# Performance work log

Hardware: AMD Instinct MI355X
Metric: run time of the kernel (lower is better)

## Reference

```python
import jax, jax.numpy as jnp
import numpy as np

D_MODEL = 1024
NUM_HEADS = 16
HEAD_DIM = D_MODEL // NUM_HEADS
THETA = 10000.0
BATCH, SEQ = 2, 2048


def rope(x, token_positions):
    # x: [b, h, s, d]; token_positions: [s]
    d = x.shape[-1]
    freqs = 1.0 / THETA ** (jnp.arange(0, d, 2, dtype=jnp.float32)[: d // 2] / d)
    ang = token_positions.astype(jnp.float32)[:, None] * freqs[None, :]  # [s, d/2]
    cos, sin = jnp.cos(ang), jnp.sin(ang)
    xr = x.reshape(*x.shape[:-1], d // 2, 2)
    x_even, x_odd = xr[..., 0], xr[..., 1]
    out_even = x_even * cos - x_odd * sin
    out_odd = x_even * sin + x_odd * cos
    return jnp.stack([out_even, out_odd], axis=-1).reshape(x.shape)


def setup_inputs() -> dict:
    key = jax.random.key(0)
    ks = jax.random.split(key, 5)
    std = np.sqrt(2.0 / (D_MODEL + D_MODEL))
    mk = lambda k: (jax.random.truncated_normal(k, -3.0, 3.0, (D_MODEL, D_MODEL), jnp.float32) * std)
    return {
        "x": jax.random.normal(ks[0], (BATCH, SEQ, D_MODEL), jnp.float32),
        "Wq": mk(ks[1]),
        "Wk": mk(ks[2]),
        "Wv": mk(ks[3]),
        "Wo": mk(ks[4]),
        "casual_mask": jnp.tril(jnp.ones((SEQ, SEQ), dtype=bool)),
        "token_positions": jnp.arange(SEQ, dtype=jnp.int32),
    }


def reference(x, Wq, Wk, Wv, Wo, casual_mask, token_positions):
    b, s, _ = x.shape
    split = lambda t: t.reshape(b, s, NUM_HEADS, HEAD_DIM).transpose(0, 2, 1, 3)
    q = split(x @ Wq.T)  # [b, h, s, d]
    k = split(x @ Wk.T)
    v = split(x @ Wv.T)
    q = rope(q, token_positions)
    k = rope(k, token_positions)
    scores = jnp.einsum("bhqd,bhkd->bhqk", q, k) / np.sqrt(HEAD_DIM)
    scores = jnp.where(casual_mask, scores, -jnp.inf)
    probs = jax.nn.softmax(scores, axis=-1)
    out = jnp.einsum("bhqk,bhkd->bhqd", probs, v)
    out = out.transpose(0, 2, 1, 3).reshape(b, s, D_MODEL)
    return out @ Wo.T
```

## Files before the change

kernel.cpp:

```cpp
#include <hip/hip_runtime.h>
#include <hip/hip_bf16.h>

#define SEQ_LEN 2048
#define NBATCH 2
#define DM 1024
#define NH 16
#define HD 64
#define NR (NBATCH * SEQ_LEN)
#define NQKV (3 * DM)
#define LDQK 2048

typedef __attribute__((ext_vector_type(8))) short bf16x8;
typedef __attribute__((ext_vector_type(4))) float f32x4;

__device__ __forceinline__ short f2b(float f) {
    __hip_bfloat16 h = __float2bfloat16(f);
    return *reinterpret_cast<short*>(&h);
}
__device__ __forceinline__ float b2f(short s) {
    union { unsigned u; float f; } x;
    x.u = ((unsigned)(unsigned short)s) << 16;
    return x.f;
}

__device__ __forceinline__ void gload_lds16(const void* g, void* l) {
    __builtin_amdgcn_global_load_lds(
        (const __attribute__((address_space(1))) unsigned int*)g,
        (__attribute__((address_space(3))) unsigned int*)l, 16, 0, 0);
}

__global__ __launch_bounds__(256) void cvt_all(
    const float* __restrict__ x,  const float* __restrict__ wq,
    const float* __restrict__ wk, const float* __restrict__ wv,
    const float* __restrict__ wo,
    __hip_bfloat16* __restrict__ xb, __hip_bfloat16* __restrict__ wqkvb,
    __hip_bfloat16* __restrict__ wob) {
    int id = blockIdx.x;
    const float* src; __hip_bfloat16* dst;
    if (id < 4096) { src = x + (size_t)id * 1024; dst = xb + (size_t)id * 1024; }
    else {
        int k = id - 4096, seg = k >> 10;
        size_t off = (size_t)(k & 1023) * 1024;
        if      (seg == 0) { src = wq + off; dst = wqkvb + off; }
        else if (seg == 1) { src = wk + off; dst = wqkvb + (1u << 20) + off; }
        else if (seg == 2) { src = wv + off; dst = wqkvb + (2u << 20) + off; }
        else               { src = wo + off; dst = wob + off; }
    }
    int i = threadIdx.x * 4;
    float4 v = *(const float4*)(src + i);
    dst[i + 0] = __float2bfloat16(v.x);
    dst[i + 1] = __float2bfloat16(v.y);
    dst[i + 2] = __float2bfloat16(v.z);
    dst[i + 3] = __float2bfloat16(v.w);
}

__device__ __forceinline__ void store_c(float* p, float v) { *p = v; }
__device__ __forceinline__ void store_c(__hip_bfloat16* p, float v) {
    *p = __float2bfloat16(v);
}

template <typename CT, bool FUSED>
__global__ __launch_bounds__(256) void gemm128(
    const __hip_bfloat16* __restrict__ A,
    const __hip_bfloat16* __restrict__ B,
    CT* __restrict__ C, int K, int ldc,
    __hip_bfloat16* __restrict__ Vtg) {
    __shared__ __hip_bfloat16 As[128 * 32];
    __shared__ __hip_bfloat16 Bs[128 * 32];
    const int t    = threadIdx.x;
    const int wave = t >> 6;
    const int lane = t & 63;
    const int quad = lane >> 4;
    const int l16  = lane & 15;
    const int wy = wave >> 1, wx = wave & 1;
    const int m0 = blockIdx.x * 128, n0 = blockIdx.y * 128;

    const int r0 = wave * 32 + (lane >> 2);
    const int c0 = (lane & 3) * 8;
    const __hip_bfloat16* Ag0 = A + (size_t)(m0 + r0) * K + c0;
    const __hip_bfloat16* Ag1 = Ag0 + (size_t)16 * K;
    const __hip_bfloat16* Bg0 = B + (size_t)(n0 + r0) * K + c0;
    const __hip_bfloat16* Bg1 = Bg0 + (size_t)16 * K;
    __hip_bfloat16* lA0 = &As[r0 * 32 + c0];
    __hip_bfloat16* lA1 = &As[(r0 + 16) * 32 + c0];
    __hip_bfloat16* lB0 = &Bs[r0 * 32 + c0];
    __hip_bfloat16* lB1 = &Bs[(r0 + 16) * 32 + c0];

    f32x4 acc[4][4];
#pragma unroll
    for (int i = 0; i < 4; i++)
#pragma unroll
        for (int j = 0; j < 4; j++) acc[i][j] = (f32x4){0.f, 0.f, 0.f, 0.f};

    for (int k0 = 0; k0 < K; k0 += 32) {
        __syncthreads();
        gload_lds16(Ag0 + k0, lA0);
        gload_lds16(Ag1 + k0, lA1);
        gload_lds16(Bg0 + k0, lB0);
        gload_lds16(Bg1 + k0, lB1);
        __syncthreads();

        bf16x8 af[4], bfr[4];
#pragma unroll
        for (int rb = 0; rb < 4; rb++)
            af[rb] = *(const bf16x8*)&As[(wy * 64 + rb * 16 + l16) * 32 + quad * 8];
#pragma unroll
        for (int cb = 0; cb < 4; cb++)
            bfr[cb] = *(const bf16x8*)&Bs[(wx * 64 + cb * 16 + l16) * 32 + quad * 8];
#pragma unroll
        for (int rb = 0; rb < 4; rb++)
#pragma unroll
            for (int cb = 0; cb < 4; cb++)
                acc[rb][cb] = __builtin_amdgcn_mfma_f32_16x16x32_bf16(
                    af[rb], bfr[cb], acc[rb][cb], 0, 0, 0);
    }

    if (!FUSED || blockIdx.y < 16) {
#pragma unroll
        for (int rb = 0; rb < 4; rb++)
#pragma unroll
            for (int r = 0; r < 4; r++) {
                size_t ro = (size_t)(m0 + wy * 64 + rb * 16 + quad * 4 + r) * ldc;
#pragma unroll
                for (int cb = 0; cb < 4; cb++)
                    store_c(&C[ro + n0 + wx * 64 + cb * 16 + l16], acc[rb][cb][r]);
            }
    } else {
#pragma unroll
        for (int rb = 0; rb < 4; rb++) {
            int row0 = m0 + wy * 64 + rb * 16 + quad * 4;
            int bb = row0 >> 11, ss = row0 & (SEQ_LEN - 1);
#pragma unroll
            for (int cb = 0; cb < 4; cb++) {
                int vcol = n0 + wx * 64 + cb * 16 + l16 - 2048;
                int hh = vcol >> 6, dd = vcol & 63;
                ushort4 u;
                u.x = (unsigned short)f2b(acc[rb][cb][0]);
                u.y = (unsigned short)f2b(acc[rb][cb][1]);
                u.z = (unsigned short)f2b(acc[rb][cb][2]);
                u.w = (unsigned short)f2b(acc[rb][cb][3]);
                *(ushort4*)(Vtg + ((size_t)(bb * NH + hh) * HD + dd) * SEQ_LEN + ss) = u;
            }
        }
    }
}

__global__ __launch_bounds__(256) void rope_kernel(
    __hip_bfloat16* __restrict__ QK, const int* __restrict__ pos) {
    int idx = blockIdx.x * 256 + threadIdx.x;
    int row  = idx >> 8;
    int tcol = idx & 255;
    int col0 = tcol * 8;
    int head = col0 >> 6;
    int i0   = (col0 & 63) >> 1;
    float p  = (float)pos[row & (SEQ_LEN - 1)];
    float scale = (head < NH) ? 0.125f : 1.0f;
    __hip_bfloat16* ptr = QK + (size_t)row * LDQK + col0;
    bf16x8 v = *(const bf16x8*)ptr;
    bf16x8 o;
#pragma unroll
    for (int k = 0; k < 4; k++) {
        float fr = __expf(-(float)(2 * (i0 + k)) * (9.210340371976184f / 64.0f));
        float ang = p * fr;
        float sn = sinf(ang), cs = cosf(ang);
        float e  = b2f(v[2 * k]);
        float od = b2f(v[2 * k + 1]);
        o[2 * k]     = f2b((e * cs - od * sn) * scale);
        o[2 * k + 1] = f2b((e * sn + od * cs) * scale);
    }
    *(bf16x8*)ptr = o;
}

__global__ __launch_bounds__(512) void attn_kernel(
    const __hip_bfloat16* __restrict__ QK,
    const __hip_bfloat16* __restrict__ Vtg,
    __hip_bfloat16* __restrict__ O) {
    __shared__ __hip_bfloat16 Ks[2][64 * 64];
    __shared__ __hip_bfloat16 Vs[2][64 * 64];
    __shared__ short Ps[128][72];

    const int t    = threadIdx.x;
    const int wave = t >> 6;
    const int lane = t & 63;
    const int quad = lane >> 4;
    const int l16  = lane & 15;
    const int pairIdx = blockIdx.x >> 5;
    const int hb      = blockIdx.x & 31;
    const int h       = hb & 15;
    const int b       = hb >> 4;

    const int sr  = t >> 3;
    const int scs = (t & 7) ^ (sr & 7);

    const __hip_bfloat16* kbase = QK + (size_t)(b * SEQ_LEN) * LDQK + DM + h * HD;
    const __hip_bfloat16* vbase = Vtg + (size_t)((b * NH + h) * HD) * SEQ_LEN;

#define STAGE(BUF, KT)                                                          \
    {                                                                           \
        gload_lds16(kbase + (size_t)((KT) * 64 + sr) * LDQK + scs * 8,          \
                    (char*)&Ks[BUF][0] + t * 16);                               \
        gload_lds16(vbase + (size_t)sr * SEQ_LEN + (KT) * 64 + scs * 8,         \
                    (char*)&Vs[BUF][0] + t * 16);                               \
    }

#define LDS_FRAG(BASE, RR, G)                                                   \
    (*(const bf16x8*)((const char*)(BASE) + (RR) * 128 + ((((G) ^ ((RR) & 7))) << 4)))

#define TRIP(BUF, KT)                                                           \
    {                                                                           \
        bf16x8 kf[4][2];                                                        \
        _Pragma("unroll") for (int kb = 0; kb < 4; kb++) {                      \
            int rr = kb * 16 + l16;                                             \
            kf[kb][0] = LDS_FRAG(Ks[BUF], rr, quad);                            \
            kf[kb][1] = LDS_FRAG(Ks[BUF], rr, quad + 4);                        \
        }                                                                       \
        f32x4 s[4];                                                             \
        _Pragma("unroll") for (int kb = 0; kb < 4; kb++) {                      \
            f32x4 z = {0.f, 0.f, 0.f, 0.f};                                     \
            z = __builtin_amdgcn_mfma_f32_16x16x32_bf16(qf0, kf[kb][0], z, 0, 0, 0); \
            z = __builtin_amdgcn_mfma_f32_16x16x32_bf16(qf1, kf[kb][1], z, 0, 0, 0); \
            s[kb] = z;                                                          \
        }                                                                       \
        if ((KT) == ktd) {                \
            _Pragma("unroll") for (int kb = 0; kb < 4; kb++) {                  \
                int key = (KT) * 64 + kb * 16 + l16;                            \
                _Pragma("unroll") for (int r = 0; r < 4; r++) {                 \
                    int rowg = row0 + quad * 4 + r;                             \
                    if (key > rowg) s[kb][r] = -1e30f;                          \
                }                                                               \
            }                                                                   \
        }                                                                       \
        _Pragma("unroll") for (int r = 0; r < 4; r++) {                         \
            float p0 = __expf(s[0][r]);                                         \
            float p1 = __expf(s[1][r]);                                         \
            float p2 = __expf(s[2][r]);                                         \
            float p3 = __expf(s[3][r]);                                         \
            l_p[r] += (p0 + p1) + (p2 + p3);                                    \
            int prow = wave * 16 + quad * 4 + r;                                \
            Ps[prow][ 0 + l16] = f2b(p0);                                       \
            Ps[prow][16 + l16] = f2b(p1);                                       \
            Ps[prow][32 + l16] = f2b(p2);                                       \
            Ps[prow][48 + l16] = f2b(p3);                                       \
        }                                                                       \
        bf16x8 pf0 = *(const bf16x8*)&Ps[wave * 16 + l16][quad * 8];            \
        bf16x8 pf1 = *(const bf16x8*)&Ps[wave * 16 + l16][32 + quad * 8];       \
        _Pragma("unroll") for (int db = 0; db < 4; db++) {                      \
            int rr = db * 16 + l16;                                             \
            bf16x8 vf0 = LDS_FRAG(Vs[BUF], rr, quad);                           \
            bf16x8 vf1 = LDS_FRAG(Vs[BUF], rr, quad + 4);                       \
            o[db] = __builtin_amdgcn_mfma_f32_16x16x32_bf16(pf0, vf0, o[db], 0, 0, 0); \
            o[db] = __builtin_amdgcn_mfma_f32_16x16x32_bf16(pf1, vf1, o[db], 0, 0, 0); \
        }                                                                       \
    }

#define FINALIZE()                                                              \
    {                                                                           \
        _Pragma("unroll") for (int r = 0; r < 4; r++) {                         \
            float rs = l_p[r];                                                  \
            rs += __shfl_xor(rs, 1);                                            \
            rs += __shfl_xor(rs, 2);                                            \
            rs += __shfl_xor(rs, 4);                                            \
            rs += __shfl_xor(rs, 8);                                            \
            float inv = 1.0f / rs;                                              \
            size_t ro = (size_t)(b * SEQ_LEN + row0 + quad * 4 + r) * DM + h * HD; \
            O[ro +  0 + l16] = __float2bfloat16(o[0][r] * inv);                 \
            O[ro + 16 + l16] = __float2bfloat16(o[1][r] * inv);                 \
            O[ro + 32 + l16] = __float2bfloat16(o[2][r] * inv);                 \
            O[ro + 48 + l16] = __float2bfloat16(o[3][r] * inv);                 \
        }                                                                       \
    }

    const int qtB = 15 - pairIdx;
    const int n0t = 2 * qtB + 2;

    int row0 = qtB * 128 + wave * 16;
    int ktd  = row0 >> 6;
    bf16x8 qf0, qf1;
    {
        const __hip_bfloat16* qp =
            QK + (size_t)(b * SEQ_LEN + row0 + l16) * LDQK + h * HD + quad * 8;
        qf0 = *(const bf16x8*)qp;
        qf1 = *(const bf16x8*)(qp + 32);
    }
    f32x4 o[4];
    float l_p[4];
#pragma unroll
    for (int r = 0; r < 4; r++) { o[r] = (f32x4){0.f, 0.f, 0.f, 0.f}; l_p[r] = 0.f; }

    STAGE(0, 0);
    for (int i = 0; i < 34; ++i) {
        const int buf = i & 1;
        __syncthreads();
        if (i + 1 < 34) {
            int inext = i + 1;
            int ktn = (inext < n0t) ? inext : inext - n0t;
            STAGE(buf ^ 1, ktn);
        }
        const int kt = (i < n0t) ? i : i - n0t;
        if (kt <= ktd) TRIP(buf, kt);
        if (i == n0t - 1) {
            FINALIZE();
            row0 = pairIdx * 128 + wave * 16;
            ktd  = row0 >> 6;
            const __hip_bfloat16* qp =
                QK + (size_t)(b * SEQ_LEN + row0 + l16) * LDQK + h * HD + quad * 8;
            qf0 = *(const bf16x8*)qp;
            qf1 = *(const bf16x8*)(qp + 32);
#pragma unroll
            for (int r = 0; r < 4; r++) { o[r] = (f32x4){0.f, 0.f, 0.f, 0.f}; l_p[r] = 0.f; }
        }
    }
    FINALIZE();
#undef STAGE
#undef LDS_FRAG
#undef TRIP
#undef FINALIZE
}

extern "C" void kernel_launch(void* const* d_in, const int* in_sizes, int n_in,
                              void* d_out, int out_size, void* d_ws, size_t ws_size,
                              hipStream_t stream) {
    const float* x  = (const float*)d_in[0];
    const float* Wq = (const float*)d_in[1];
    const float* Wk = (const float*)d_in[2];
    const float* Wv = (const float*)d_in[3];
    const float* Wo = (const float*)d_in[4];
    const int* pos = (const int*)d_in[6];
    float* out = (float*)d_out;

    char* w = (char*)d_ws;
    const size_t MiB = 1024 * 1024;
    __hip_bfloat16* xb    = (__hip_bfloat16*)(w + 0 * MiB);
    __hip_bfloat16* Ab    = (__hip_bfloat16*)(w + 0 * MiB);
    __hip_bfloat16* Wqkvb = (__hip_bfloat16*)(w + 8 * MiB);
    __hip_bfloat16* Wob   = (__hip_bfloat16*)(w + 14 * MiB);
    __hip_bfloat16* QKb   = (__hip_bfloat16*)(w + 16 * MiB);
    __hip_bfloat16* Vtg   = (__hip_bfloat16*)(w + 32 * MiB);

    cvt_all<<<8192, 256, 0, stream>>>(x, Wq, Wk, Wv, Wo, xb, Wqkvb, Wob);

    gemm128<__hip_bfloat16, true><<<dim3(NR / 128, NQKV / 128), 256, 0, stream>>>(
        xb, Wqkvb, QKb, DM, LDQK, Vtg);

    rope_kernel<<<NR * LDQK / 8 / 256, 256, 0, stream>>>(QKb, pos);

    attn_kernel<<<256, 512, 0, stream>>>(QKb, Vtg, Ab);

    gemm128<float, false><<<dim3(NR / 128, DM / 128), 256, 0, stream>>>(
        Ab, Wob, out, DM, DM, nullptr);
}
```

Before: 211.8 us.

## Fuse RoPE into QKV GEMM epilogue and restructure attention into 64-row tiles

Applies RoPE and the query scale inside the QKV GEMM epilogue, using a lane shuffle to fetch the paired element, and deletes the separate rope kernel along with its read and write of the QK buffer. The attention kernel changes from 256 blocks of 512 threads, each handling a paired 128-row tile, to 1024 blocks of 256 threads, each handling one 64-row query tile with heaviest tiles scheduled first. It also wraps the MFMA sections in s_setprio hints. The risks are extra sincos work and shuffles in the GEMM epilogue, and load imbalance from dropping the tile pairing, which the larger grid is meant to absorb.

```diff
diff --git a/kernel.cpp b/kernel.cpp
--- a/kernel.cpp
+++ b/kernel.cpp
@@ -64,7 +64,7 @@
     const __hip_bfloat16* __restrict__ A,
     const __hip_bfloat16* __restrict__ B,
     CT* __restrict__ C, int K, int ldc,
-    __hip_bfloat16* __restrict__ Vtg) {
+    __hip_bfloat16* __restrict__ Vtg, const int* __restrict__ pos) {
     __shared__ __hip_bfloat16 As[128 * 32];
     __shared__ __hip_bfloat16 Bs[128 * 32];
     const int t    = threadIdx.x;
@@ -116,6 +116,31 @@
     }
 
     if (!FUSED || blockIdx.y < 16) {
+        if constexpr (FUSED) {
+            const float sc = (blockIdx.y < 8) ? 0.125f : 1.0f;
+            float fr[4];
+#pragma unroll
+            for (int cb = 0; cb < 4; cb++) {
+                int i = ((cb * 16 + l16) & 63) >> 1;
+                fr[cb] = __expf(-(float)(2 * i) * (9.210340371976184f / 64.0f));
+            }
+            const float par = (l16 & 1) ? 1.f : -1.f;
+#pragma unroll
+            for (int rb = 0; rb < 4; rb++)
+#pragma unroll
+                for (int r = 0; r < 4; r++) {
+                    int row = m0 + wy * 64 + rb * 16 + quad * 4 + r;
+                    float p = (float)pos[row & (SEQ_LEN - 1)];
+#pragma unroll
+                    for (int cb = 0; cb < 4; cb++) {
+                        float sn, cs;
+                        __sincosf(p * fr[cb], &sn, &cs);
+                        float v  = acc[rb][cb][r];
+                        float pt = __shfl_xor(v, 1);
+                        acc[rb][cb][r] = (v * cs + par * pt * sn) * sc;
+                    }
+                }
+        }
 #pragma unroll
         for (int rb = 0; rb < 4; rb++)
 #pragma unroll
@@ -145,49 +170,26 @@
     }
 }
 
-__global__ __launch_bounds__(256) void rope_kernel(
-    __hip_bfloat16* __restrict__ QK, const int* __restrict__ pos) {
-    int idx = blockIdx.x * 256 + threadIdx.x;
-    int row  = idx >> 8;
-    int tcol = idx & 255;
-    int col0 = tcol * 8;
-    int head = col0 >> 6;
-    int i0   = (col0 & 63) >> 1;
-    float p  = (float)pos[row & (SEQ_LEN - 1)];
-    float scale = (head < NH) ? 0.125f : 1.0f;
-    __hip_bfloat16* ptr = QK + (size_t)row * LDQK + col0;
-    bf16x8 v = *(const bf16x8*)ptr;
-    bf16x8 o;
-#pragma unroll
-    for (int k = 0; k < 4; k++) {
-        float fr = __expf(-(float)(2 * (i0 + k)) * (9.210340371976184f / 64.0f));
-        float ang = p * fr;
-        float sn = sinf(ang), cs = cosf(ang);
-        float e  = b2f(v[2 * k]);
-        float od = b2f(v[2 * k + 1]);
-        o[2 * k]     = f2b((e * cs - od * sn) * scale);
-        o[2 * k + 1] = f2b((e * sn + od * cs) * scale);
-    }
-    *(bf16x8*)ptr = o;
-}
-
-__global__ __launch_bounds__(512) void attn_kernel(
+__global__ __launch_bounds__(256) void attn_kernel(
     const __hip_bfloat16* __restrict__ QK,
     const __hip_bfloat16* __restrict__ Vtg,
     __hip_bfloat16* __restrict__ O) {
     __shared__ __hip_bfloat16 Ks[2][64 * 64];
     __shared__ __hip_bfloat16 Vs[2][64 * 64];
-    __shared__ short Ps[128][72];
+    __shared__ short Ps[64][72];
 
     const int t    = threadIdx.x;
     const int wave = t >> 6;
     const int lane = t & 63;
     const int quad = lane >> 4;
     const int l16  = lane & 15;
-    const int pairIdx = blockIdx.x >> 5;
-    const int hb      = blockIdx.x & 31;
-    const int h       = hb & 15;
-    const int b       = hb >> 4;
+    const int id  = blockIdx.x;
+    const int qt  = 31 - (id >> 5);
+    const int hb  = id & 31;
+    const int h   = hb & 15;
+    const int b   = hb >> 4;
+
+    const int row0 = qt * 64 + wave * 16;
 
     const int sr  = t >> 3;
     const int scs = (t & 7) ^ (sr & 7);
@@ -199,8 +201,12 @@
     {                                                                           \
         gload_lds16(kbase + (size_t)((KT) * 64 + sr) * LDQK + scs * 8,          \
                     (char*)&Ks[BUF][0] + t * 16);                               \
+        gload_lds16(kbase + (size_t)((KT) * 64 + sr + 32) * LDQK + scs * 8,     \
+                    (char*)&Ks[BUF][0] + (t + 256) * 16);                       \
         gload_lds16(vbase + (size_t)sr * SEQ_LEN + (KT) * 64 + scs * 8,         \
                     (char*)&Vs[BUF][0] + t * 16);                               \
+        gload_lds16(vbase + (size_t)(sr + 32) * SEQ_LEN + (KT) * 64 + scs * 8,  \
+                    (char*)&Vs[BUF][0] + (t + 256) * 16);                       \
     }
 
 #define LDS_FRAG(BASE, RR, G)                                                   \
@@ -215,13 +221,15 @@
             kf[kb][1] = LDS_FRAG(Ks[BUF], rr, quad + 4);                        \
         }                                                                       \
         f32x4 s[4];                                                             \
+        __builtin_amdgcn_s_setprio(1);                                          \
         _Pragma("unroll") for (int kb = 0; kb < 4; kb++) {                      \
             f32x4 z = {0.f, 0.f, 0.f, 0.f};                                     \
             z = __builtin_amdgcn_mfma_f32_16x16x32_bf16(qf0, kf[kb][0], z, 0, 0, 0); \
             z = __builtin_amdgcn_mfma_f32_16x16x32_bf16(qf1, kf[kb][1], z, 0, 0, 0); \
             s[kb] = z;                                                          \
         }                                                                       \
-        if ((KT) == ktd) {                \
+        __builtin_amdgcn_s_setprio(0);                                          \
+        if ((KT) == qt) {                 \
             _Pragma("unroll") for (int kb = 0; kb < 4; kb++) {                  \
                 int key = (KT) * 64 + kb * 16 + l16;                            \
                 _Pragma("unroll") for (int r = 0; r < 4; r++) {                 \
@@ -244,6 +252,7 @@
         }                                                                       \
         bf16x8 pf0 = *(const bf16x8*)&Ps[wave * 16 + l16][quad * 8];            \
         bf16x8 pf1 = *(const bf16x8*)&Ps[wave * 16 + l16][32 + quad * 8];       \
+        __builtin_amdgcn_s_setprio(1);                                          \
         _Pragma("unroll") for (int db = 0; db < 4; db++) {                      \
             int rr = db * 16 + l16;                                             \
             bf16x8 vf0 = LDS_FRAG(Vs[BUF], rr, quad);                           \
@@ -251,30 +260,9 @@
             o[db] = __builtin_amdgcn_mfma_f32_16x16x32_bf16(pf0, vf0, o[db], 0, 0, 0); \
             o[db] = __builtin_amdgcn_mfma_f32_16x16x32_bf16(pf1, vf1, o[db], 0, 0, 0); \
         }                                                                       \
-    }
-
-#define FINALIZE()                                                              \
-    {                                                                           \
-        _Pragma("unroll") for (int r = 0; r < 4; r++) {                         \
-            float rs = l_p[r];                                                  \
-            rs += __shfl_xor(rs, 1);                                            \
-            rs += __shfl_xor(rs, 2);                                            \
-            rs += __shfl_xor(rs, 4);                                            \
-            rs += __shfl_xor(rs, 8);                                            \
-            float inv = 1.0f / rs;                                              \
-            size_t ro = (size_t)(b * SEQ_LEN + row0 + quad * 4 + r) * DM + h * HD; \
-            O[ro +  0 + l16] = __float2bfloat16(o[0][r] * inv);                 \
-            O[ro + 16 + l16] = __float2bfloat16(o[1][r] * inv);                 \
-            O[ro + 32 + l16] = __float2bfloat16(o[2][r] * inv);                 \
-            O[ro + 48 + l16] = __float2bfloat16(o[3][r] * inv);                 \
-        }                                                                       \
-    }
-
-    const int qtB = 15 - pairIdx;
-    const int n0t = 2 * qtB + 2;
-
-    int row0 = qtB * 128 + wave * 16;
-    int ktd  = row0 >> 6;
+        __builtin_amdgcn_s_setprio(0);                                          \
+    }
+
     bf16x8 qf0, qf1;
     {
         const __hip_bfloat16* qp =
@@ -288,33 +276,30 @@
     for (int r = 0; r < 4; r++) { o[r] = (f32x4){0.f, 0.f, 0.f, 0.f}; l_p[r] = 0.f; }
 
     STAGE(0, 0);
-    for (int i = 0; i < 34; ++i) {
-        const int buf = i & 1;
+    for (int kt = 0; kt <= qt; ++kt) {
+        const int buf = kt & 1;
         __syncthreads();
-        if (i + 1 < 34) {
-            int inext = i + 1;
-            int ktn = (inext < n0t) ? inext : inext - n0t;
-            STAGE(buf ^ 1, ktn);
-        }
-        const int kt = (i < n0t) ? i : i - n0t;
-        if (kt <= ktd) TRIP(buf, kt);
-        if (i == n0t - 1) {
-            FINALIZE();
-            row0 = pairIdx * 128 + wave * 16;
-            ktd  = row0 >> 6;
-            const __hip_bfloat16* qp =
-                QK + (size_t)(b * SEQ_LEN + row0 + l16) * LDQK + h * HD + quad * 8;
-            qf0 = *(const bf16x8*)qp;
-            qf1 = *(const bf16x8*)(qp + 32);
-#pragma unroll
-            for (int r = 0; r < 4; r++) { o[r] = (f32x4){0.f, 0.f, 0.f, 0.f}; l_p[r] = 0.f; }
-        }
-    }
-    FINALIZE();
+        if (kt < qt) STAGE(buf ^ 1, kt + 1);
+        TRIP(buf, kt);
+    }
+
+#pragma unroll
+    for (int r = 0; r < 4; r++) {
+        float rs = l_p[r];
+        rs += __shfl_xor(rs, 1);
+        rs += __shfl_xor(rs, 2);
+        rs += __shfl_xor(rs, 4);
+        rs += __shfl_xor(rs, 8);
+        float inv = 1.0f / rs;
+        size_t ro = (size_t)(b * SEQ_LEN + row0 + quad * 4 + r) * DM + h * HD;
+        O[ro +  0 + l16] = __float2bfloat16(o[0][r] * inv);
+        O[ro + 16 + l16] = __float2bfloat16(o[1][r] * inv);
+        O[ro + 32 + l16] = __float2bfloat16(o[2][r] * inv);
+        O[ro + 48 + l16] = __float2bfloat16(o[3][r] * inv);
+    }
 #undef STAGE
 #undef LDS_FRAG
 #undef TRIP
-#undef FINALIZE
 }
 
 extern "C" void kernel_launch(void* const* d_in, const int* in_sizes, int n_in,
@@ -340,12 +325,10 @@
     cvt_all<<<8192, 256, 0, stream>>>(x, Wq, Wk, Wv, Wo, xb, Wqkvb, Wob);
 
     gemm128<__hip_bfloat16, true><<<dim3(NR / 128, NQKV / 128), 256, 0, stream>>>(
-        xb, Wqkvb, QKb, DM, LDQK, Vtg);
-
-    rope_kernel<<<NR * LDQK / 8 / 256, 256, 0, stream>>>(QKb, pos);
-
-    attn_kernel<<<256, 512, 0, stream>>>(QKb, Vtg, Ab);
+        xb, Wqkvb, QKb, DM, LDQK, Vtg, pos);
+
+    attn_kernel<<<1024, 256, 0, stream>>>(QKb, Vtg, Ab);
 
     gemm128<float, false><<<dim3(NR / 128, DM / 128), 256, 0, stream>>>(
-        Ab, Wob, out, DM, DM, nullptr);
-}
+        Ab, Wob, out, DM, DM, nullptr, nullptr);
+}
```

New measurement: 198.6 us. -6.2%, faster.
